# Kernel tuning notes

Measured on AMD Instinct MI355X. Metric: run time of the kernel, lower is better.

Reference implementation:

```python
import jax, jax.numpy as jnp
import numpy as np

B, L, KD, ED, H = 8, 4096, 512, 1024, 8  # batch, seq, key_dim, embed_dim, n_heads
LN_EPS = 1e-5


def setup_inputs() -> dict:
    key = jax.random.key(0)
    ks = jax.random.split(key, 6)
    keys = jax.random.normal(ks[0], (B, L, KD), dtype=jnp.float32)
    values = jax.random.normal(ks[1], (B, L, ED), dtype=jnp.float32)
    # learned params
    query = jax.random.normal(ks[2], (H, 1, KD // H), dtype=jnp.float32) * 0.02
    k_bias = jax.random.normal(ks[3], (KD,), dtype=jnp.float32) / np.sqrt(KD).astype(np.float32)
    v_bias = jnp.zeros((ED,), dtype=jnp.float32)
    softmax_weight = 1.0 + 0.01 * jax.random.normal(ks[4], (H, 1, L + 1), dtype=jnp.float32)
    softmax_bias = 0.01 * jax.random.normal(ks[5], (H, 1, L + 1), dtype=jnp.float32)
    gamma = jnp.ones((ED,), dtype=jnp.float32)
    beta = jnp.zeros((ED,), dtype=jnp.float32)
    return {"keys": keys, "values": values, "query": query, "k_bias": k_bias,
            "v_bias": v_bias, "softmax_weight": softmax_weight,
            "softmax_bias": softmax_bias, "gamma": gamma, "beta": beta}


def reference(keys, values, query, k_bias, v_bias, softmax_weight, softmax_bias, gamma, beta):
    b = keys.shape[0]
    # append learned bias token to keys and values  -> [B, L+1, *]
    keys = jnp.concatenate([keys, jnp.broadcast_to(k_bias, (b, 1, k_bias.shape[0]))], axis=1)
    values = jnp.concatenate([values, jnp.broadcast_to(v_bias, (b, 1, v_bias.shape[0]))], axis=1)
    lp = keys.shape[1]
    # torch multihead_reshape is a raw contiguous view [B,L,C] -> [B*H, L, C/H]
    K = keys.reshape(b * H, lp, keys.shape[2] // H)      # [B*H, L+1, KD/H]
    V = values.reshape(b * H, lp, values.shape[2] // H)  # [B*H, L+1, ED/H]
    Q = jnp.tile(query, (b, 1, 1))                       # [B*H, 1, KD/H]
    scores = jnp.einsum('bqd,bld->bql', Q, K)            # [B*H, 1, L+1]
    scores = scores * jnp.tile(softmax_weight, (b, 1, 1)) + jnp.tile(softmax_bias, (b, 1, 1))
    attn = jax.nn.softmax(scores, axis=-1)               # [B*H, 1, L+1]
    A = jnp.einsum('bql,bld->bqd', attn, V)              # [B*H, 1, ED/H]
    A = A.reshape(b, 1, -1)                              # multihead_unshape -> [B, 1, ED]
    # LayerNorm over embed dim (torch default eps=1e-5, biased var)
    mean = jnp.mean(A, axis=-1, keepdims=True)
    var = jnp.var(A, axis=-1, keepdims=True)
    return (A - mean) * jax.lax.rsqrt(var + LN_EPS) * gamma + beta
```

## Files before the change

### kernel.cpp

```cpp
#include <hip/hip_runtime.h>
#include <hip/hip_bf16.h>

#define BATCH 8
#define LSEQ  4096
#define LP    4097
#define KDIM  512
#define EDIM  1024
#define NH    8
#define DK    64
#define DV    128
#define NG    (BATCH*NH)
#define SSTR  4112
#define NC    16
#define RC    257
#define LN_EPS 1e-5f


__global__ __launch_bounds__(256) void scores_kernel(
    const float* __restrict__ keys, const float* __restrict__ k_bias,
    const float* __restrict__ query, float* __restrict__ p)
{
    const int chunk = blockIdx.x;
    const int g = blockIdx.y;
    const int b = g >> 3, h = g & 7;
    const int t = threadIdx.x;
    const int lane16 = t & 15;
    const int d0 = lane16 * 4;

    const float4 q = *reinterpret_cast<const float4*>(query + h * DK + d0);

    const float* kp = keys + (long long)b * (LSEQ * KDIM);
    const int fhead = h * (LP * DK);
    const int row0 = chunk * 513;
    const int row_end = min(LP, row0 + 513);
    float* prow = p + (long long)g * SSTR;

    for (int row = row0 + (t >> 4); row < row_end; row += 16) {
        const int f = fhead + row * DK + d0;
        const float4 k = (f < LSEQ * KDIM)
                       ? *reinterpret_cast<const float4*>(kp + f)
                       : *reinterpret_cast<const float4*>(k_bias + (f - LSEQ * KDIM));
        float s = q.x * k.x + q.y * k.y + q.z * k.z + q.w * k.w;
        s += __shfl_xor(s, 1);
        s += __shfl_xor(s, 2);
        s += __shfl_xor(s, 4);
        s += __shfl_xor(s, 8);
        if (lane16 == 0) prow[row] = s;
    }
}

__global__ __launch_bounds__(256) void softmax_kernel(
    const float* __restrict__ sw, const float* __restrict__ sb,
    float* __restrict__ p, float* __restrict__ Z)
{
    const int g = blockIdx.x;
    const int h = g & 7;
    const int t = threadIdx.x;
    float* prow = p + (long long)g * SSTR;
    const float* w = sw + h * LP;
    const float* bb = sb + h * LP;
    __shared__ float red[256];

    float m = -1e30f;
    for (int j = t; j < LP; j += 256)
        m = fmaxf(m, prow[j] * w[j] + bb[j]);
    red[t] = m; __syncthreads();
    for (int off = 128; off > 0; off >>= 1) {
        if (t < off) red[t] = fmaxf(red[t], red[t + off]);
        __syncthreads();
    }
    m = red[0];
    __syncthreads();

    float z = 0.f;
    for (int j = t; j < LP; j += 256) {
        float e = __expf(prow[j] * w[j] + bb[j] - m);
        prow[j] = e;
        z += e;
    }
    red[t] = z; __syncthreads();
    for (int off = 128; off > 0; off >>= 1) {
        if (t < off) red[t] += red[t + off];
        __syncthreads();
    }
    if (t == 0) Z[g] = red[0];
}

__global__ __launch_bounds__(256) void av_kernel(
    const float* __restrict__ values, const float* __restrict__ v_bias,
    const float* __restrict__ p, float* __restrict__ partials)
{
    const int chunk = blockIdx.x;
    const int g = blockIdx.y;
    const int b = g >> 3, h = g & 7;
    const int t = threadIdx.x;
    const int srow = t >> 5;
    const int d0 = (t & 31) * 4;

    const float* vp = values + (long long)b * (LSEQ * EDIM);
    const int fhead = h * (LP * DV);
    const float* prow = p + (long long)g * SSTR;
    const int row0 = chunk * RC;
    const int row_end = min(LP, row0 + RC);

    float acc[4] = {0.f, 0.f, 0.f, 0.f};
    for (int row = row0 + srow; row < row_end; row += 8) {
        const float pw = prow[row];
        const int f = fhead + row * DV + d0;
        const float4 v = (f < LSEQ * EDIM)
                       ? *reinterpret_cast<const float4*>(vp + f)
                       : *reinterpret_cast<const float4*>(v_bias + (f - LSEQ * EDIM));
        acc[0] += pw * v.x; acc[1] += pw * v.y;
        acc[2] += pw * v.z; acc[3] += pw * v.w;
    }

    __shared__ float red[256 * 4];
#pragma unroll
    for (int j = 0; j < 4; ++j) red[t * 4 + j] = acc[j];
    for (int off = 128; off >= 32; off >>= 1) {
        __syncthreads();
        if (t < off) {
#pragma unroll
            for (int j = 0; j < 4; ++j) red[t * 4 + j] += red[(t + off) * 4 + j];
        }
    }
    __syncthreads();
    if (t < 32) {
        float* dst = partials + ((long long)(g * NC + chunk)) * DV + t * 4;
#pragma unroll
        for (int j = 0; j < 4; ++j) dst[j] = red[t * 4 + j];
    }
}

__global__ __launch_bounds__(256) void ln_kernel(
    const float* __restrict__ partials, const float* __restrict__ Z,
    const float* __restrict__ gamma, const float* __restrict__ beta,
    float* __restrict__ out)
{
    const int b = blockIdx.x;
    const int t = threadIdx.x;
    __shared__ float r1[256], r2[256];

    float a[4];
    float s1 = 0.f, s2 = 0.f;
#pragma unroll
    for (int i = 0; i < 4; ++i) {
        const int e = t + i * 256;
        const int h = e >> 7, d = e & 127;
        const float* src = partials + ((long long)((b * NH + h) * NC)) * DV + d;
        float sum = 0.f;
#pragma unroll
        for (int c = 0; c < NC; ++c) sum += src[c * DV];
        const float av = sum / Z[b * NH + h];
        a[i] = av;
        s1 += av;
        s2 += av * av;
    }
    r1[t] = s1; r2[t] = s2; __syncthreads();
    for (int off = 128; off > 0; off >>= 1) {
        if (t < off) { r1[t] += r1[t + off]; r2[t] += r2[t + off]; }
        __syncthreads();
    }
    const float mean = r1[0] * (1.0f / EDIM);
    const float var = r2[0] * (1.0f / EDIM) - mean * mean;
    const float inv = rsqrtf(var + LN_EPS);
#pragma unroll
    for (int i = 0; i < 4; ++i) {
        const int e = t + i * 256;
        out[(long long)b * EDIM + e] =
            (a[i] - mean) * inv * gamma[e] + beta[e];
    }
}

extern "C" void kernel_launch(void* const* d_in, const int* in_sizes, int n_in,
                              void* d_out, int out_size, void* d_ws, size_t ws_size,
                              hipStream_t stream) {
    const float* keys   = (const float*)d_in[0];
    const float* values = (const float*)d_in[1];
    const float* query  = (const float*)d_in[2];
    const float* k_bias = (const float*)d_in[3];
    const float* v_bias = (const float*)d_in[4];
    const float* sw     = (const float*)d_in[5];
    const float* sb     = (const float*)d_in[6];
    const float* gamma  = (const float*)d_in[7];
    const float* beta   = (const float*)d_in[8];
    float* out = (float*)d_out;

    float* ws = (float*)d_ws;
    float* p = ws;
    float* Z = ws + (long long)NG * SSTR;
    float* partials = Z + NG;

    scores_kernel <<<dim3(8, NG),  256, 0, stream>>>(keys, k_bias, query, p);
    softmax_kernel<<<NG,           256, 0, stream>>>(sw, sb, p, Z);
    av_kernel     <<<dim3(NC, NG), 256, 0, stream>>>(values, v_bias, p, partials);
    ln_kernel     <<<BATCH,        256, 0, stream>>>(partials, Z, gamma, beta, out);
}
```

Baseline: 270.3 us.

## Fuse softmax into scores via online max/sum stats, normalize in AV kernel

The separate softmax kernel is removed. The scores kernel now applies the softmax weight and bias and keeps a per-chunk online max and exp-sum, which it writes as float2 stats. The AV kernel merges the chunk stats, computes normalized probabilities into shared memory, and uses nontemporal loads for values and keys. This drops one launch and an extra pass over the score buffer, in exchange for redundant exp work in every AV block and serial online-softmax updates in the lane-0 threads.

```diff
diff --git a/kernel.cpp b/kernel.cpp
--- a/kernel.cpp
+++ b/kernel.cpp
@@ -1,5 +1,4 @@
 #include <hip/hip_runtime.h>
-#include <hip/hip_bf16.h>
 
 #define BATCH 8
 #define LSEQ  4096
@@ -9,16 +8,21 @@
 #define NH    8
 #define DK    64
 #define DV    128
-#define NG    (BATCH*NH)
+#define NG    64
 #define SSTR  4112
+#define NCK   8
+#define RCK   513
 #define NC    16
 #define RC    257
 #define LN_EPS 1e-5f
 
-
-__global__ __launch_bounds__(256) void scores_kernel(
+typedef float floatx4 __attribute__((ext_vector_type(4)));
+
+__global__ __launch_bounds__(256) void lqa_scores_kernel(
     const float* __restrict__ keys, const float* __restrict__ k_bias,
-    const float* __restrict__ query, float* __restrict__ p)
+    const float* __restrict__ query, const float* __restrict__ sw,
+    const float* __restrict__ sb, float* __restrict__ p,
+    float2* __restrict__ stats)
 {
     const int chunk = blockIdx.x;
     const int g = blockIdx.y;
@@ -27,68 +31,55 @@
     const int lane16 = t & 15;
     const int d0 = lane16 * 4;
 
-    const float4 q = *reinterpret_cast<const float4*>(query + h * DK + d0);
-
+    const floatx4 q = *reinterpret_cast<const floatx4*>(query + h * DK + d0);
     const float* kp = keys + (long long)b * (LSEQ * KDIM);
     const int fhead = h * (LP * DK);
-    const int row0 = chunk * 513;
-    const int row_end = min(LP, row0 + 513);
+    const int row0 = chunk * RCK;
+    const int row_end = min(LP, row0 + RCK);
     float* prow = p + (long long)g * SSTR;
-
+    const float* w = sw + h * LP;
+    const float* bb = sb + h * LP;
+
+    float mloc = -1e30f, zloc = 0.f;
     for (int row = row0 + (t >> 4); row < row_end; row += 16) {
         const int f = fhead + row * DK + d0;
-        const float4 k = (f < LSEQ * KDIM)
-                       ? *reinterpret_cast<const float4*>(kp + f)
-                       : *reinterpret_cast<const float4*>(k_bias + (f - LSEQ * KDIM));
+        floatx4 k;
+        if (f < LSEQ * KDIM)
+            k = __builtin_nontemporal_load(reinterpret_cast<const floatx4*>(kp + f));
+        else
+            k = *reinterpret_cast<const floatx4*>(k_bias + (f - LSEQ * KDIM));
         float s = q.x * k.x + q.y * k.y + q.z * k.z + q.w * k.w;
         s += __shfl_xor(s, 1);
         s += __shfl_xor(s, 2);
         s += __shfl_xor(s, 4);
         s += __shfl_xor(s, 8);
-        if (lane16 == 0) prow[row] = s;
-    }
-}
-
-__global__ __launch_bounds__(256) void softmax_kernel(
-    const float* __restrict__ sw, const float* __restrict__ sb,
-    float* __restrict__ p, float* __restrict__ Z)
-{
-    const int g = blockIdx.x;
-    const int h = g & 7;
-    const int t = threadIdx.x;
-    float* prow = p + (long long)g * SSTR;
-    const float* w = sw + h * LP;
-    const float* bb = sb + h * LP;
-    __shared__ float red[256];
-
-    float m = -1e30f;
-    for (int j = t; j < LP; j += 256)
-        m = fmaxf(m, prow[j] * w[j] + bb[j]);
-    red[t] = m; __syncthreads();
+        if (lane16 == 0) {
+            const float tv = s * w[row] + bb[row];
+            prow[row] = tv;
+            if (tv > mloc) { zloc = zloc * __expf(mloc - tv) + 1.f; mloc = tv; }
+            else            zloc += __expf(tv - mloc);
+        }
+    }
+
+    __shared__ float mred[256], zred[256];
+    mred[t] = mloc; zred[t] = zloc;
     for (int off = 128; off > 0; off >>= 1) {
-        if (t < off) red[t] = fmaxf(red[t], red[t + off]);
         __syncthreads();
-    }
-    m = red[0];
-    __syncthreads();
-
-    float z = 0.f;
-    for (int j = t; j < LP; j += 256) {
-        float e = __expf(prow[j] * w[j] + bb[j] - m);
-        prow[j] = e;
-        z += e;
-    }
-    red[t] = z; __syncthreads();
-    for (int off = 128; off > 0; off >>= 1) {
-        if (t < off) red[t] += red[t + off];
-        __syncthreads();
-    }
-    if (t == 0) Z[g] = red[0];
-}
-
-__global__ __launch_bounds__(256) void av_kernel(
+        if (t < off) {
+            const float m1 = mred[t], z1 = zred[t];
+            const float m2 = mred[t + off], z2 = zred[t + off];
+            const float m = fmaxf(m1, m2);
+            mred[t] = m;
+            zred[t] = z1 * __expf(m1 - m) + z2 * __expf(m2 - m);
+        }
+    }
+    if (t == 0) stats[g * NCK + chunk] = make_float2(mred[0], zred[0]);
+}
+
+__global__ __launch_bounds__(256) void lqa_av_kernel(
     const float* __restrict__ values, const float* __restrict__ v_bias,
-    const float* __restrict__ p, float* __restrict__ partials)
+    const float* __restrict__ p, const float2* __restrict__ stats,
+    float* __restrict__ partials)
 {
     const int chunk = blockIdx.x;
     const int g = blockIdx.y;
@@ -97,21 +88,38 @@
     const int srow = t >> 5;
     const int d0 = (t & 31) * 4;
 
+    float m = -1e30f, Z = 0.f;
+#pragma unroll
+    for (int c = 0; c < NCK; ++c) {
+        const float2 s = stats[g * NCK + c];
+        const float mn = fmaxf(m, s.x);
+        Z = Z * __expf(m - mn) + s.y * __expf(s.x - mn);
+        m = mn;
+    }
+    const float rinv = 1.f / Z;
+
     const float* vp = values + (long long)b * (LSEQ * EDIM);
     const int fhead = h * (LP * DV);
     const float* prow = p + (long long)g * SSTR;
     const int row0 = chunk * RC;
-    const int row_end = min(LP, row0 + RC);
+    const int nrows = min(LP, row0 + RC) - row0;
+
+    __shared__ float pw[RC];
+    for (int r = t; r < nrows; r += 256)
+        pw[r] = __expf(prow[row0 + r] - m) * rinv;
+    __syncthreads();
 
     float acc[4] = {0.f, 0.f, 0.f, 0.f};
-    for (int row = row0 + srow; row < row_end; row += 8) {
-        const float pw = prow[row];
-        const int f = fhead + row * DV + d0;
-        const float4 v = (f < LSEQ * EDIM)
-                       ? *reinterpret_cast<const float4*>(vp + f)
-                       : *reinterpret_cast<const float4*>(v_bias + (f - LSEQ * EDIM));
-        acc[0] += pw * v.x; acc[1] += pw * v.y;
-        acc[2] += pw * v.z; acc[3] += pw * v.w;
+    for (int r = srow; r < nrows; r += 8) {
+        const float wgt = pw[r];
+        const int f = fhead + (row0 + r) * DV + d0;
+        floatx4 v;
+        if (f < LSEQ * EDIM)
+            v = __builtin_nontemporal_load(reinterpret_cast<const floatx4*>(vp + f));
+        else
+            v = *reinterpret_cast<const floatx4*>(v_bias + (f - LSEQ * EDIM));
+        acc[0] += wgt * v.x; acc[1] += wgt * v.y;
+        acc[2] += wgt * v.z; acc[3] += wgt * v.w;
     }
 
     __shared__ float red[256 * 4];
@@ -132,10 +140,9 @@
     }
 }
 
-__global__ __launch_bounds__(256) void ln_kernel(
-    const float* __restrict__ partials, const float* __restrict__ Z,
-    const float* __restrict__ gamma, const float* __restrict__ beta,
-    float* __restrict__ out)
+__global__ __launch_bounds__(256) void lqa_ln_kernel(
+    const float* __restrict__ partials, const float* __restrict__ gamma,
+    const float* __restrict__ beta, float* __restrict__ out)
 {
     const int b = blockIdx.x;
     const int t = threadIdx.x;
@@ -151,10 +158,9 @@
         float sum = 0.f;
 #pragma unroll
         for (int c = 0; c < NC; ++c) sum += src[c * DV];
-        const float av = sum / Z[b * NH + h];
-        a[i] = av;
-        s1 += av;
-        s2 += av * av;
+        a[i] = sum;
+        s1 += sum;
+        s2 += sum * sum;
     }
     r1[t] = s1; r2[t] = s2; __syncthreads();
     for (int off = 128; off > 0; off >>= 1) {
@@ -167,8 +173,7 @@
 #pragma unroll
     for (int i = 0; i < 4; ++i) {
         const int e = t + i * 256;
-        out[(long long)b * EDIM + e] =
-            (a[i] - mean) * inv * gamma[e] + beta[e];
+        out[(long long)b * EDIM + e] = (a[i] - mean) * inv * gamma[e] + beta[e];
     }
 }
 
@@ -188,11 +193,10 @@
 
     float* ws = (float*)d_ws;
     float* p = ws;
-    float* Z = ws + (long long)NG * SSTR;
-    float* partials = Z + NG;
-
-    scores_kernel <<<dim3(8, NG),  256, 0, stream>>>(keys, k_bias, query, p);
-    softmax_kernel<<<NG,           256, 0, stream>>>(sw, sb, p, Z);
-    av_kernel     <<<dim3(NC, NG), 256, 0, stream>>>(values, v_bias, p, partials);
-    ln_kernel     <<<BATCH,        256, 0, stream>>>(partials, Z, gamma, beta, out);
-}
+    float2* stats = (float2*)(ws + (long long)NG * SSTR);
+    float* partials = ws + (long long)NG * SSTR + NG * NCK * 2;
+
+    lqa_scores_kernel<<<dim3(NCK, NG), 256, 0, stream>>>(keys, k_bias, query, sw, sb, p, stats);
+    lqa_av_kernel    <<<dim3(NC, NG),  256, 0, stream>>>(values, v_bias, p, stats, partials);
+    lqa_ln_kernel    <<<BATCH,         256, 0, stream>>>(partials, gamma, beta, out);
+}
```

After: 278.6 us. 1.03x slower.
